# Kernel optimization log

Hardware: AMD Instinct MI355X
Metric: run time of the kernel (lower is better)

The kernel has to match this reference:

```python
import jax, jax.numpy as jnp
import numpy as np
import math

HEAD_DIM = 64
NQ = 24          # num query heads
NKV = 4          # num kv heads
HIDDEN = 1536
WINDOW = 256     # sliding window (layer_idx=0 -> active)
THETA = 10000.0
EPS = 1e-6


def _rope(x, cos, sin):
    # x: [B,S,H,D]; cos/sin: [S,1,D//2]  (broadcast over B and heads)
    xr = x.reshape(*x.shape[:-1], -1, 2)
    x1, x2 = xr[..., 0], xr[..., 1]
    r = jnp.stack([x1 * cos - x2 * sin, x2 * cos + x1 * sin], axis=-1)
    return r.reshape(x.shape)


def setup_inputs() -> dict:
    key = jax.random.key(0)
    k1, k2, k3 = jax.random.split(key, 3)
    B, S = 2, 2048
    x = jax.random.normal(k1, (B, S, HIDDEN), dtype=jnp.float32)
    norm_scale = jnp.ones((HIDDEN,), dtype=jnp.float32)             # RMSNorm scale
    w_qkv = jax.random.normal(k2, ((NQ + 2 * NKV) * HEAD_DIM, HIDDEN), dtype=jnp.float32) * 0.02
    w_out = jax.random.normal(k3, (HIDDEN, NQ * HEAD_DIM), dtype=jnp.float32) * 0.02
    return {"x": x, "norm_scale": norm_scale, "w_qkv": w_qkv, "w_out": w_out, "start_pos": 0}


def reference(x, norm_scale, w_qkv, w_out, start_pos):
    B, S, _ = x.shape
    # RMSNorm
    var = jnp.mean(x * x, axis=-1, keepdims=True)
    xn = x * jax.lax.rsqrt(var + EPS) * norm_scale
    # QKV projection (nn.Linear: x @ W^T)
    qkv = xn @ w_qkv.T
    qs, kvs = NQ * HEAD_DIM, NKV * HEAD_DIM
    q = qkv[..., :qs].reshape(B, S, NQ, HEAD_DIM)
    k = qkv[..., qs:qs + kvs].reshape(B, S, NKV, HEAD_DIM)
    v = qkv[..., qs + kvs:].reshape(B, S, NKV, HEAD_DIM)
    # RoPE
    inv_freq = 1.0 / (THETA ** (jnp.arange(0, HEAD_DIM, 2, dtype=jnp.float32) / HEAD_DIM))
    t = jnp.arange(start_pos, start_pos + S, dtype=jnp.float32)
    freqs = t[:, None] * inv_freq[None, :]                       # [S, D//2]
    cos, sin = jnp.cos(freqs)[:, None, :], jnp.sin(freqs)[:, None, :]
    q = _rope(q, cos, sin)
    k = _rope(k, cos, sin)
    # GQA: expand kv heads (repeat_interleave over head dim)
    rep = NQ // NKV
    k = jnp.repeat(k, rep, axis=2)
    v = jnp.repeat(v, rep, axis=2)
    # attention with causal + sliding-window mask
    scale = 1.0 / math.sqrt(HEAD_DIM)
    scores = jnp.einsum('bqhd,bkhd->bhqk', q * scale, k)        # [B,H,S,S]
    ipos = start_pos + jnp.arange(S)
    j = jnp.arange(S)
    mask = (j[None, :] > ipos[:, None]) | (j[None, :] < ipos[:, None] - WINDOW)
    scores = jnp.where(mask[None, None], -jnp.inf, scores)
    probs = jax.nn.softmax(scores, axis=-1)
    attn = jnp.einsum('bhqk,bkhd->bqhd', probs, v).reshape(B, S, NQ * HEAD_DIM)
    # output projection + residual
    return x + attn @ w_out.T
```

## Files before the change

kernel.cpp:

```cpp
#include <hip/hip_runtime.h>
#include <hip/hip_bf16.h>

typedef float f32x4 __attribute__((ext_vector_type(4)));
typedef short s16x8 __attribute__((ext_vector_type(8)));
typedef unsigned short u16;

#define B_ 2
#define S_ 2048
#define HID 1536
#define NQ_ 24
#define NKV_ 4
#define HD 64
#define NTOK (B_*S_)
#define QKVN ((NQ_+2*NKV_)*HD)

#define CVT_BLKS  ((QKVN*HID + HID*HID)/4/256)
#define RMS_BLKS  NTOK
#define TAB_BLKS  (S_*32/256)
#define SETUP_BLKS (CVT_BLKS + RMS_BLKS + TAB_BLKS)

#define ROPE2_BLOCKS ((NTOK*28*16)/256)
#define VT_BLOCKS (B_*NKV_*(S_/64))

#define LDS_FENCE() asm volatile("" ::: "memory")

#define WAITBAR(n) asm volatile("s_waitcnt vmcnt(" #n ")\n\ts_barrier" ::: "memory")
#define RAWBAR()   asm volatile("s_barrier" ::: "memory")

__device__ __forceinline__ float bf2f(u16 u) {
  unsigned int x = ((unsigned int)u) << 16;
  float f; __builtin_memcpy(&f, &x, 4); return f;
}
__device__ __forceinline__ u16 f2bf(float f) {
  unsigned int u; __builtin_memcpy(&u, &f, 4);
  u += 0x7fffu + ((u >> 16) & 1u);
  return (u16)(u >> 16);
}
__device__ __forceinline__ unsigned long long pk4bf(float a, float b, float c, float d) {
  __hip_bfloat162 x = __float22bfloat162_rn(make_float2(a, b));
  __hip_bfloat162 y = __float22bfloat162_rn(make_float2(c, d));
  unsigned int xi, yi;
  __builtin_memcpy(&xi, &x, 4);
  __builtin_memcpy(&yi, &y, 4);
  return (unsigned long long)xi | ((unsigned long long)yi << 32);
}

__global__ __launch_bounds__(256) void k_setup(const float* __restrict__ x,
                                               const float* __restrict__ g,
                                               const float* __restrict__ wq,
                                               const float* __restrict__ wo,
                                               u16* __restrict__ wb,
                                               u16* __restrict__ xn,
                                               float2* __restrict__ tab,
                                               const int* __restrict__ spp) {
  int bid = blockIdx.x, tid = threadIdx.x;
  if (bid < CVT_BLKS) {
    int i = bid * 256 + tid;
    const int n0q = QKVN*HID/4;
    const float* src = (i < n0q) ? wq : wo;
    int j = (i < n0q) ? i : i - n0q;
    f32x4 v = ((const f32x4*)src)[j];
    *(unsigned long long*)(wb + (size_t)i*4) = pk4bf(v[0], v[1], v[2], v[3]);
  } else if (bid < CVT_BLKS + RMS_BLKS) {
    int row = bid - CVT_BLKS;
    const f32x4* xr = (const f32x4*)(x + (size_t)row * HID);
    f32x4 v0 = {}, v1 = {};
    float ss = 0.f;
    if (tid < 192) {
      v0 = xr[2*tid]; v1 = xr[2*tid + 1];
      ss = v0[0]*v0[0] + v0[1]*v0[1] + v0[2]*v0[2] + v0[3]*v0[3]
         + v1[0]*v1[0] + v1[1]*v1[1] + v1[2]*v1[2] + v1[3]*v1[3];
    }
#pragma unroll
    for (int off = 1; off < 64; off <<= 1) ss += __shfl_xor(ss, off);
    __shared__ float red[4];
    if ((tid & 63) == 0) red[tid >> 6] = ss;
    __syncthreads();
    float rs = rsqrtf((red[0] + red[1] + red[2] + red[3]) * (1.f/HID) + 1e-6f);
    if (tid < 192) {
      const f32x4* gr = (const f32x4*)g;
      f32x4 g0 = gr[2*tid], g1 = gr[2*tid + 1];
      unsigned long long* out = (unsigned long long*)(xn + (size_t)row * HID);
      out[2*tid]     = pk4bf(v0[0]*rs*g0[0], v0[1]*rs*g0[1], v0[2]*rs*g0[2], v0[3]*rs*g0[3]);
      out[2*tid + 1] = pk4bf(v1[0]*rs*g1[0], v1[1]*rs*g1[1], v1[2]*rs*g1[2], v1[3]*rs*g1[3]);
    }
  } else {
    int i = (bid - CVT_BLKS - RMS_BLKS) * 256 + tid;
    int s = i >> 5, p = i & 31;
    float t = (float)(spp[0] + s);
    float inv = exp2f((float)p * -0.41524101186f);
    float sn, cs;
    sincosf(t * inv, &sn, &cs);
    tab[i] = make_float2(cs, sn);
  }
}

template <bool F32OUT>
__global__ __launch_bounds__(256) void k_gemm_bt(const u16* __restrict__ A,
                                                 const u16* __restrict__ W,
                                                 void* __restrict__ Cv,
                                                 const float* __restrict__ resid,
                                                 int N, int K) {
  __shared__ __align__(16) u16 As0[128*64], Bs0[64*64];
  __shared__ __align__(16) u16 As1[128*64], Bs1[64*64];
  int lin = blockIdx.x;
  int xcd = lin & 7, loc = lin >> 3;
  int mloc = loc & 3, nloc = loc >> 2;
  int m0 = (xcd*4 + mloc) * 128, n0 = nloc * 64;
  int tid = threadIdx.x;
  int w = tid >> 6, l = tid & 63;
  int wr = w >> 1, wc = w & 1;
  int c = l & 15, g = l >> 4;
  f32x4 acc[4][2] = {};
  int r8 = l >> 3;
  int sslot = (l & 7) ^ r8;
  const u16* Ag = A + (size_t)(m0 + w*32 + r8)*K + sslot*8;
  const u16* Wg = W + (size_t)(n0 + w*16 + r8)*K + sslot*8;

#define STAGE(dA, dB, k0) do {                                                          \
  _Pragma("unroll")                                                                     \
  for (int i = 0; i < 4; i++)                                                           \
    __builtin_amdgcn_global_load_lds(                                                   \
        (const __attribute__((address_space(1))) void*)(Ag + (size_t)(i*8)*K + (k0)),   \
        (__attribute__((address_space(3))) void*)(dA + (w*32 + i*8)*64), 16, 0, 0);     \
  _Pragma("unroll")                                                                     \
  for (int i = 0; i < 2; i++)                                                           \
    __builtin_amdgcn_global_load_lds(                                                   \
        (const __attribute__((address_space(1))) void*)(Wg + (size_t)(i*8)*K + (k0)),   \
        (__attribute__((address_space(3))) void*)(dB + (w*16 + i*8)*64), 16, 0, 0);     \
  } while (0)

#define COMPUTE(sA, sB) do {                                                            \
  _Pragma("unroll")                                                                     \
  for (int ks = 0; ks < 2; ks++) {                                                      \
    s16x8 af[4], bq[2];                                                                 \
    int sl = ((ks*4 + g) ^ (c & 7)) * 8;                                                \
    _Pragma("unroll")                                                                   \
    for (int mt = 0; mt < 4; mt++)                                                      \
      af[mt] = *(const s16x8*)(sA + (wr*64 + mt*16 + c)*64 + sl);                       \
    _Pragma("unroll")                                                                   \
    for (int nt = 0; nt < 2; nt++)                                                      \
      bq[nt] = *(const s16x8*)(sB + (wc*32 + nt*16 + c)*64 + sl);                       \
    _Pragma("unroll")                                                                   \
    for (int mt = 0; mt < 4; mt++)                                                      \
      _Pragma("unroll")                                                                 \
      for (int nt = 0; nt < 2; nt++)                                                    \
        acc[mt][nt] = __builtin_amdgcn_mfma_f32_16x16x32_bf16(af[mt], bq[nt],           \
                                                              acc[mt][nt], 0, 0, 0);    \
  } } while (0)

  const int NT = K >> 6;
  STAGE(As0, Bs0, 0);
  STAGE(As1, Bs1, 64);
  WAITBAR(6);
  for (int t = 0; t + 2 < NT; t += 2) {
    COMPUTE(As0, Bs0);
    RAWBAR();
    STAGE(As0, Bs0, (t+2)*64);
    WAITBAR(6);
    COMPUTE(As1, Bs1);
    RAWBAR();
    if (t + 3 < NT) {
      STAGE(As1, Bs1, (t+3)*64);
      WAITBAR(6);
    } else {
      WAITBAR(0);
    }
  }
  COMPUTE(As0, Bs0);
  WAITBAR(0);
  COMPUTE(As1, Bs1);
#undef STAGE
#undef COMPUTE

#pragma unroll
  for (int mt = 0; mt < 4; mt++)
#pragma unroll
    for (int nt = 0; nt < 2; nt++)
#pragma unroll
      for (int r = 0; r < 4; r++) {
        int m = m0 + wr*64 + mt*16 + g*4 + r;
        int n = n0 + wc*32 + nt*16 + c;
        size_t off = (size_t)m*N + n;
        float vv = acc[mt][nt][r];
        if (F32OUT) {
          ((float*)Cv)[off] = vv + resid[off];
        } else {
          ((u16*)Cv)[off] = f2bf(vv);
        }
      }
}

__global__ __launch_bounds__(256) void k_rope_vt(const u16* __restrict__ qkv,
                                                 u16* __restrict__ q,
                                                 u16* __restrict__ k,
                                                 u16* __restrict__ vt,
                                                 const float2* __restrict__ tab) {
  __shared__ u16 tile[64][65];
  int bid = blockIdx.x;
  if (bid < ROPE2_BLOCKS) {
    int idx = bid * 256 + threadIdx.x;
    int j = idx & 15;
    int h = (idx >> 4) % 28;
    int tok = idx / 448;
    int s = tok & (S_ - 1);
    int b = tok >> 11;
    f32x4 cs = *(const f32x4*)(tab + (size_t)s*32 + 2*j);
    int col = (h < NQ_) ? h*64 + 4*j : HID + (h - NQ_)*64 + 4*j;
    unsigned long long pr = *(const unsigned long long*)(qkv + (size_t)tok*QKVN + col);
    float x1a = bf2f((u16)pr),         x2a = bf2f((u16)(pr >> 16));
    float x1b = bf2f((u16)(pr >> 32)), x2b = bf2f((u16)(pr >> 48));
    float ya1 = x1a*cs[0] - x2a*cs[1];
    float ya2 = x2a*cs[0] + x1a*cs[1];
    float yb1 = x1b*cs[2] - x2b*cs[3];
    float yb2 = x2b*cs[2] + x1b*cs[3];
    unsigned long long outp = pk4bf(ya1, ya2, yb1, yb2);
    if (h < NQ_) {
      *(unsigned long long*)(q + (((size_t)(b*NQ_ + h))*S_ + s)*64 + 4*j) = outp;
    } else {
      *(unsigned long long*)(k + (((size_t)(b*NKV_ + (h - NQ_)))*S_ + s)*64 + 4*j) = outp;
    }
  } else {
    int blk = bid - ROPE2_BLOCKS;
    int st = blk & 31;
    int hk = (blk >> 5) & 3;
    int b = blk >> 7;
    int s0 = st * 64;
#pragma unroll
    for (int i = 0; i < 16; i++) {
      int ii = threadIdx.x + i*256;
      int r = ii >> 6, cc = ii & 63;
      tile[r][cc] = qkv[((size_t)(b*S_) + s0 + r)*QKVN + (NQ_+NKV_)*64 + hk*64 + cc];
    }
    __syncthreads();
#pragma unroll
    for (int i = 0; i < 16; i++) {
      int ii = threadIdx.x + i*256;
      int d = ii >> 6, s = ii & 63;
      vt[((size_t)(b*NKV_ + hk)*64 + d)*S_ + s0 + s] = tile[s][d];
    }
  }
}

__global__ __launch_bounds__(64, 3) void k_attn(const u16* __restrict__ q,
                                                const u16* __restrict__ k,
                                                const u16* __restrict__ vt,
                                                u16* __restrict__ ao,
                                                const int* __restrict__ spp) {
  __shared__ __align__(16) u16 Pt[32*72];
  int lin = blockIdx.x;
  int xcd = lin & 7, loc = lin >> 3;
  int qb = loc & 63;
  int bh = xcd * 6 + (loc >> 6);
  int h = bh % NQ_;
  int b = bh / NQ_;
  int q0 = qb * 32;
  int hk = h / (NQ_/NKV_);
  int l = threadIdx.x;
  int c = l & 15, g = l >> 4;
  int sp = spp[0];
  const u16* qptr = q + ((size_t)(b*NQ_ + h))*S_*64;
  const u16* kptr = k + ((size_t)(b*NKV_ + hk))*S_*64;
  const u16* vptr = vt + ((size_t)(b*NKV_ + hk))*64*S_;

  s16x8 qf[2][2];
#pragma unroll
  for (int qt = 0; qt < 2; qt++)
#pragma unroll
    for (int ks = 0; ks < 2; ks++)
      qf[qt][ks] = *(const s16x8*)(qptr + (size_t)(q0 + qt*16 + c)*64 + ks*32 + g*8);

  f32x4 o[4][2] = {};
  float m_run[2], l_run[2];
#pragma unroll
  for (int i = 0; i < 2; i++) { m_run[i] = -1e30f; l_run[i] = 0.f; }

  int lo = sp + q0 - 256; if (lo < 0) lo = 0;
  int hi = sp + q0 + 31;  if (hi > S_ - 1) hi = S_ - 1;
  int kt0 = lo >> 6, kt1 = hi >> 6;

  s16x8 kf[4][2];
#pragma unroll
  for (int km = 0; km < 4; km++)
#pragma unroll
    for (int ks = 0; ks < 2; ks++)
      kf[km][ks] = *(const s16x8*)(kptr + (size_t)(kt0*64 + km*16 + c)*64 + ks*32 + g*8);

  for (int kt = kt0; kt <= kt1; kt++) {
    s16x8 vf[2][4];
#pragma unroll
    for (int ks = 0; ks < 2; ks++)
#pragma unroll
      for (int dt = 0; dt < 4; dt++)
        vf[ks][dt] = *(const s16x8*)(vptr + (size_t)(dt*16 + c)*S_ + kt*64 + ks*32 + g*8);

    bool full = (kt*64 + 63 <= sp + q0) && (kt*64 >= sp + q0 - 225);
#pragma unroll
    for (int qt = 0; qt < 2; qt++) {
      f32x4 sa[4];
      __builtin_amdgcn_s_setprio(1);
#pragma unroll
      for (int km = 0; km < 4; km++) {
        f32x4 z = {};
        z = __builtin_amdgcn_mfma_f32_16x16x32_bf16(kf[km][0], qf[qt][0], z, 0, 0, 0);
        sa[km] = __builtin_amdgcn_mfma_f32_16x16x32_bf16(kf[km][1], qf[qt][1], z, 0, 0, 0);
      }
      __builtin_amdgcn_s_setprio(0);
      if (qt == 1 && kt < kt1) {
#pragma unroll
        for (int km = 0; km < 4; km++)
#pragma unroll
          for (int ks = 0; ks < 2; ks++)
            kf[km][ks] = *(const s16x8*)(kptr + (size_t)((kt+1)*64 + km*16 + c)*64 + ks*32 + g*8);
      }
      float mx = -1e30f;
      if (full) {
#pragma unroll
        for (int km = 0; km < 4; km++)
#pragma unroll
          for (int r = 0; r < 4; r++) {
            float sv = sa[km][r] * 0.125f;
            sa[km][r] = sv;
            mx = fmaxf(mx, sv);
          }
      } else {
        int pos = sp + q0 + qt*16 + c;
#pragma unroll
        for (int km = 0; km < 4; km++)
#pragma unroll
          for (int r = 0; r < 4; r++) {
            int key = kt*64 + km*16 + g*4 + r;
            float sv = sa[km][r] * 0.125f;
            sv = ((unsigned)(pos - key) <= 256u) ? sv : -1e30f;
            sa[km][r] = sv;
            mx = fmaxf(mx, sv);
          }
      }
      mx = fmaxf(mx, __shfl_xor(mx, 16));
      mx = fmaxf(mx, __shfl_xor(mx, 32));
      if (__ballot(mx > m_run[qt] + 8.f) != 0) {
        float mnew = fmaxf(m_run[qt], mx);
        float alpha = __expf(m_run[qt] - mnew);
        m_run[qt] = mnew;
        l_run[qt] *= alpha;
#pragma unroll
        for (int dt = 0; dt < 4; dt++) {
          o[dt][qt][0] *= alpha; o[dt][qt][1] *= alpha;
          o[dt][qt][2] *= alpha; o[dt][qt][3] *= alpha;
        }
      }
      float mref = m_run[qt];
      float rsum = 0.f;
#pragma unroll
      for (int km = 0; km < 4; km++) {
        float p0 = __expf(sa[km][0] - mref);
        float p1 = __expf(sa[km][1] - mref);
        float p2 = __expf(sa[km][2] - mref);
        float p3 = __expf(sa[km][3] - mref);
        rsum += p0 + p1 + p2 + p3;
        *(unsigned long long*)(Pt + (qt*16 + c)*72 + km*16 + g*4) = pk4bf(p0, p1, p2, p3);
      }
      rsum += __shfl_xor(rsum, 16);
      rsum += __shfl_xor(rsum, 32);
      l_run[qt] += rsum;
    }
    LDS_FENCE();
    __builtin_amdgcn_s_setprio(1);
#pragma unroll
    for (int ks = 0; ks < 2; ks++)
#pragma unroll
      for (int qt = 0; qt < 2; qt++) {
        s16x8 pf = *(const s16x8*)(Pt + (qt*16 + c)*72 + ks*32 + g*8);
#pragma unroll
        for (int dt = 0; dt < 4; dt++)
          o[dt][qt] = __builtin_amdgcn_mfma_f32_16x16x32_bf16(vf[ks][dt], pf, o[dt][qt], 0, 0, 0);
      }
    __builtin_amdgcn_s_setprio(0);
    LDS_FENCE();
  }
#pragma unroll
  for (int qt = 0; qt < 2; qt++) {
    float inv = 1.f / l_run[qt];
    int qi = q0 + qt*16 + c;
    u16* row = ao + ((size_t)(b*S_) + qi)*HID + h*64;
#pragma unroll
    for (int dt = 0; dt < 4; dt++)
      *(unsigned long long*)(row + dt*16 + g*4) =
          pk4bf(o[dt][qt][0]*inv, o[dt][qt][1]*inv, o[dt][qt][2]*inv, o[dt][qt][3]*inv);
  }
}

extern "C" void kernel_launch(void* const* d_in, const int* in_sizes, int n_in,
                              void* d_out, int out_size, void* d_ws, size_t ws_size,
                              hipStream_t stream) {
  const float* x_f32    = (const float*)d_in[0];
  const float* g_f32    = (const float*)d_in[1];
  const float* wqkv_f32 = (const float*)d_in[2];
  const float* wout_f32 = (const float*)d_in[3];
  const int*   spp      = (const int*)d_in[4];
  char* ws = (char*)d_ws;
  u16* wqkvb = (u16*)(ws);
  u16* woutb = (u16*)(ws + 6291456);
  u16* xn    = (u16*)(ws + 11010048);
  u16* qkv   = (u16*)(ws + 23592960);
  u16* qbuf  = (u16*)(ws + 40370176);
  u16* kbuf  = (u16*)(ws + 52953088);
  u16* vtb   = (u16*)(ws + 55050240);
  u16* attn  = xn;
  float2* tab = (float2*)d_out;

  k_setup<<<SETUP_BLKS, 256, 0, stream>>>(x_f32, g_f32, wqkv_f32, wout_f32,
                                          wqkvb, xn, tab, spp);
  k_gemm_bt<false><<<32*(QKVN/64), 256, 0, stream>>>(xn, wqkvb, qkv, nullptr, QKVN, HID);
  k_rope_vt<<<ROPE2_BLOCKS + VT_BLOCKS, 256, 0, stream>>>(qkv, qbuf, kbuf, vtb,
                                                          (const float2*)tab);
  k_attn<<<B_*NQ_*(S_/32), 64, 0, stream>>>(qbuf, kbuf, vtb, attn, spp);
  k_gemm_bt<true><<<32*(HID/64), 256, 0, stream>>>(attn, woutb, d_out, x_f32, HID, HID);
}
```

Measured before the change: 202.9 us.

## Fuse RoPE and V-transpose into QKV GEMM epilogue, drop intermediate qkv buffer

The QKV projection GEMM now applies rotary embedding in its epilogue, using a lane shuffle to get each element's pair partner, and writes Q and K straight into their head-major layouts. V is written already transposed. This removes the separate rope/transpose kernel and one round trip of the qkv intermediate through global memory. In exchange, the epilogue stores are scattered 2-byte writes for Q and K, and it adds per-element table loads and extra register pressure.

```diff
diff --git a/kernel.cpp b/kernel.cpp
--- a/kernel.cpp
+++ b/kernel.cpp
@@ -18,9 +18,6 @@
 #define RMS_BLKS  NTOK
 #define TAB_BLKS  (S_*32/256)
 #define SETUP_BLKS (CVT_BLKS + RMS_BLKS + TAB_BLKS)
-
-#define ROPE2_BLOCKS ((NTOK*28*16)/256)
-#define VT_BLOCKS (B_*NKV_*(S_/64))
 
 #define LDS_FENCE() asm volatile("" ::: "memory")
 
@@ -95,11 +92,15 @@
   }
 }
 
-template <bool F32OUT>
+template <int MODE>
 __global__ __launch_bounds__(256) void k_gemm_bt(const u16* __restrict__ A,
                                                  const u16* __restrict__ W,
                                                  void* __restrict__ Cv,
                                                  const float* __restrict__ resid,
+                                                 const float2* __restrict__ tab,
+                                                 u16* __restrict__ qp,
+                                                 u16* __restrict__ kp,
+                                                 u16* __restrict__ vp,
                                                  int N, int K) {
   __shared__ __align__(16) u16 As0[128*64], Bs0[64*64];
   __shared__ __align__(16) u16 As1[128*64], Bs1[64*64];
@@ -176,70 +177,52 @@
 #pragma unroll
   for (int mt = 0; mt < 4; mt++)
 #pragma unroll
-    for (int nt = 0; nt < 2; nt++)
-#pragma unroll
-      for (int r = 0; r < 4; r++) {
-        int m = m0 + wr*64 + mt*16 + g*4 + r;
+    for (int nt = 0; nt < 2; nt++) {
+      if (MODE == 1) {
+#pragma unroll
+        for (int r = 0; r < 4; r++) {
+          int m = m0 + wr*64 + mt*16 + g*4 + r;
+          int n = n0 + wc*32 + nt*16 + c;
+          size_t off = (size_t)m*N + n;
+          ((float*)Cv)[off] = acc[mt][nt][r] + resid[off];
+        }
+      } else {
         int n = n0 + wc*32 + nt*16 + c;
-        size_t off = (size_t)m*N + n;
-        float vv = acc[mt][nt][r];
-        if (F32OUT) {
-          ((float*)Cv)[off] = vv + resid[off];
+        int d = n & 63;
+        f32x4 px;
+#pragma unroll
+        for (int r = 0; r < 4; r++) px[r] = __shfl_xor(acc[mt][nt][r], 1);
+        if (n < NQ_*HD) {
+          int h = n >> 6;
+#pragma unroll
+          for (int r = 0; r < 4; r++) {
+            int m = m0 + wr*64 + mt*16 + g*4 + r;
+            int s = m & (S_-1), bb = m >> 11;
+            float2 t2 = tab[s*32 + (d >> 1)];
+            float y = (n & 1) ? acc[mt][nt][r]*t2.x + px[r]*t2.y
+                              : acc[mt][nt][r]*t2.x - px[r]*t2.y;
+            qp[(((size_t)(bb*NQ_ + h))*S_ + s)*64 + d] = f2bf(y);
+          }
+        } else if (n < (NQ_+NKV_)*HD) {
+          int hk = (n >> 6) - NQ_;
+#pragma unroll
+          for (int r = 0; r < 4; r++) {
+            int m = m0 + wr*64 + mt*16 + g*4 + r;
+            int s = m & (S_-1), bb = m >> 11;
+            float2 t2 = tab[s*32 + (d >> 1)];
+            float y = (n & 1) ? acc[mt][nt][r]*t2.x + px[r]*t2.y
+                              : acc[mt][nt][r]*t2.x - px[r]*t2.y;
+            kp[(((size_t)(bb*NKV_ + hk))*S_ + s)*64 + d] = f2bf(y);
+          }
         } else {
-          ((u16*)Cv)[off] = f2bf(vv);
+          int hk = (n >> 6) - (NQ_+NKV_);
+          int m = m0 + wr*64 + mt*16 + g*4;
+          int s = m & (S_-1), bb = m >> 11;
+          *(unsigned long long*)(vp + (((size_t)(bb*NKV_ + hk))*64 + d)*S_ + s) =
+              pk4bf(acc[mt][nt][0], acc[mt][nt][1], acc[mt][nt][2], acc[mt][nt][3]);
         }
       }
-}
-
-__global__ __launch_bounds__(256) void k_rope_vt(const u16* __restrict__ qkv,
-                                                 u16* __restrict__ q,
-                                                 u16* __restrict__ k,
-                                                 u16* __restrict__ vt,
-                                                 const float2* __restrict__ tab) {
-  __shared__ u16 tile[64][65];
-  int bid = blockIdx.x;
-  if (bid < ROPE2_BLOCKS) {
-    int idx = bid * 256 + threadIdx.x;
-    int j = idx & 15;
-    int h = (idx >> 4) % 28;
-    int tok = idx / 448;
-    int s = tok & (S_ - 1);
-    int b = tok >> 11;
-    f32x4 cs = *(const f32x4*)(tab + (size_t)s*32 + 2*j);
-    int col = (h < NQ_) ? h*64 + 4*j : HID + (h - NQ_)*64 + 4*j;
-    unsigned long long pr = *(const unsigned long long*)(qkv + (size_t)tok*QKVN + col);
-    float x1a = bf2f((u16)pr),         x2a = bf2f((u16)(pr >> 16));
-    float x1b = bf2f((u16)(pr >> 32)), x2b = bf2f((u16)(pr >> 48));
-    float ya1 = x1a*cs[0] - x2a*cs[1];
-    float ya2 = x2a*cs[0] + x1a*cs[1];
-    float yb1 = x1b*cs[2] - x2b*cs[3];
-    float yb2 = x2b*cs[2] + x1b*cs[3];
-    unsigned long long outp = pk4bf(ya1, ya2, yb1, yb2);
-    if (h < NQ_) {
-      *(unsigned long long*)(q + (((size_t)(b*NQ_ + h))*S_ + s)*64 + 4*j) = outp;
-    } else {
-      *(unsigned long long*)(k + (((size_t)(b*NKV_ + (h - NQ_)))*S_ + s)*64 + 4*j) = outp;
     }
-  } else {
-    int blk = bid - ROPE2_BLOCKS;
-    int st = blk & 31;
-    int hk = (blk >> 5) & 3;
-    int b = blk >> 7;
-    int s0 = st * 64;
-#pragma unroll
-    for (int i = 0; i < 16; i++) {
-      int ii = threadIdx.x + i*256;
-      int r = ii >> 6, cc = ii & 63;
-      tile[r][cc] = qkv[((size_t)(b*S_) + s0 + r)*QKVN + (NQ_+NKV_)*64 + hk*64 + cc];
-    }
-    __syncthreads();
-#pragma unroll
-    for (int i = 0; i < 16; i++) {
-      int ii = threadIdx.x + i*256;
-      int d = ii >> 6, s = ii & 63;
-      vt[((size_t)(b*NKV_ + hk)*64 + d)*S_ + s0 + s] = tile[s][d];
-    }
-  }
 }
 
 __global__ __launch_bounds__(64, 3) void k_attn(const u16* __restrict__ q,
@@ -402,7 +385,6 @@
   u16* wqkvb = (u16*)(ws);
   u16* woutb = (u16*)(ws + 6291456);
   u16* xn    = (u16*)(ws + 11010048);
-  u16* qkv   = (u16*)(ws + 23592960);
   u16* qbuf  = (u16*)(ws + 40370176);
   u16* kbuf  = (u16*)(ws + 52953088);
   u16* vtb   = (u16*)(ws + 55050240);
@@ -411,9 +393,11 @@
 
   k_setup<<<SETUP_BLKS, 256, 0, stream>>>(x_f32, g_f32, wqkv_f32, wout_f32,
                                           wqkvb, xn, tab, spp);
-  k_gemm_bt<false><<<32*(QKVN/64), 256, 0, stream>>>(xn, wqkvb, qkv, nullptr, QKVN, HID);
-  k_rope_vt<<<ROPE2_BLOCKS + VT_BLOCKS, 256, 0, stream>>>(qkv, qbuf, kbuf, vtb,
-                                                          (const float2*)tab);
+  k_gemm_bt<0><<<32*(QKVN/64), 256, 0, stream>>>(xn, wqkvb, nullptr, nullptr,
+                                                 (const float2*)tab, qbuf, kbuf, vtb,
+                                                 QKVN, HID);
   k_attn<<<B_*NQ_*(S_/32), 64, 0, stream>>>(qbuf, kbuf, vtb, attn, spp);
-  k_gemm_bt<true><<<32*(HID/64), 256, 0, stream>>>(attn, woutb, d_out, x_f32, HID, HID);
-}
+  k_gemm_bt<1><<<32*(HID/64), 256, 0, stream>>>(attn, woutb, d_out, x_f32,
+                                                nullptr, nullptr, nullptr, nullptr,
+                                                HID, HID);
+}
```

Measured after the change: 200.5 us. No clear change (-1.1%).
